# Kernel optimization log

Measured on AMD Instinct MI355X. Metric: run time of the kernel, lower is better.

Reference implementation:

```python
import jax, jax.numpy as jnp
import numpy as np

B, K, C = 8, 16384, 256
NPROP, NSAMPLE, RADIUS = 1024, 16, 0.3
NUM_CLASS, NH, NS = 18, 12, 18
DOUT = 2 + 3 + NH * 2 + NS * 4 + NUM_CLASS  # 119


def setup_inputs() -> dict:
    key = jax.random.key(0)
    ks = jax.random.split(key, 16)
    w = lambda k, shape: jax.random.normal(k, shape, jnp.float32) * 0.05
    return {
        "xyz": jax.random.uniform(ks[0], (B, K, 3), jnp.float32) * 4.0,
        "features": jax.random.normal(ks[1], (B, C, K), jnp.float32),
        # SA shared-MLP (conv2d 1x1) weights, BN folded to scale/bias (inference)
        "W1": w(ks[2], (128, C + 3)), "g1": jnp.ones((128,), jnp.float32), "b1": jnp.zeros((128,), jnp.float32),
        "W2": w(ks[3], (128, 128)),   "g2": jnp.ones((128,), jnp.float32), "b2": jnp.zeros((128,), jnp.float32),
        "W3": w(ks[4], (128, 128)),   "g3": jnp.ones((128,), jnp.float32), "b3": jnp.zeros((128,), jnp.float32),
        # proposal head conv1d stack
        "P1": w(ks[5], (128, 128)),  "pg1": jnp.ones((128,), jnp.float32), "pb1": jnp.zeros((128,), jnp.float32),
        "P2": w(ks[6], (128, 128)),  "pg2": jnp.ones((128,), jnp.float32), "pb2": jnp.zeros((128,), jnp.float32),
        "P3": w(ks[7], (DOUT, 128)), "pb3": jnp.zeros((DOUT,), jnp.float32),
        "mean_size_arr": jnp.abs(jax.random.normal(ks[8], (NS, 3), jnp.float32)) + 0.5,
    }


def fps(xyz, npoint):
    """Farthest point sampling. xyz: [B,K,3] -> [B,npoint] int32."""
    Bn, Kn, _ = xyz.shape
    def step(carry, _):
        dist, far = carry                                   # [B,K], [B]
        sel = jnp.take_along_axis(xyz, far[:, None, None], axis=1)  # [B,1,3]
        d = jnp.sum((xyz - sel) ** 2, axis=-1)              # [B,K]
        dist = jnp.minimum(dist, d)
        return (dist, jnp.argmax(dist, axis=-1).astype(jnp.int32)), far
    init = (jnp.full((Bn, Kn), 1e10, xyz.dtype), jnp.zeros((Bn,), jnp.int32))
    _, inds = jax.lax.scan(step, init, None, length=npoint)  # [npoint,B]
    return inds.T


def ball_query(new_xyz, xyz, radius, nsample):
    """First nsample points within radius of each center (pad with first hit)."""
    Kn = xyz.shape[1]
    d2 = jnp.sum((new_xyz[:, :, None, :] - xyz[:, None, :, :]) ** 2, axis=-1)  # [B,P,K]
    idx = jnp.where(d2 < radius * radius, jnp.arange(Kn, dtype=jnp.int32)[None, None, :], Kn)
    idx = jnp.sort(idx, axis=-1)[..., :nsample]             # first hits in index order
    first = idx[..., :1]                                    # center itself is always a hit
    return jnp.where(idx == Kn, first, idx).astype(jnp.int32)


def reference(xyz, features, W1, g1, b1, W2, g2, b2, W3, g3, b3,
              P1, pg1, pb1, P2, pg2, pb2, P3, pb3, mean_size_arr):
    Bn = xyz.shape[0]
    fps_idx = fps(xyz, NPROP)                                           # [B,P]
    new_xyz = jnp.take_along_axis(xyz, fps_idx[:, :, None], axis=1)     # [B,P,3]
    idx = ball_query(new_xyz, xyz, RADIUS, NSAMPLE)                     # [B,P,S]
    flat = idx.reshape(Bn, -1)
    g_xyz = jnp.take_along_axis(xyz, flat[:, :, None], axis=1).reshape(Bn, NPROP, NSAMPLE, 3)
    g_xyz = (g_xyz - new_xyz[:, :, None, :]) / RADIUS                   # normalize_xyz=True
    f = jnp.swapaxes(features, 1, 2)                                    # [B,K,C]
    g_feat = jnp.take_along_axis(f, flat[:, :, None], axis=1).reshape(Bn, NPROP, NSAMPLE, C)
    x = jnp.concatenate([g_xyz, g_feat], axis=-1)                       # [B,P,S,C+3] (use_xyz)
    for Wl, gl, bl in ((W1, g1, b1), (W2, g2, b2), (W3, g3, b3)):
        x = jax.nn.relu(jnp.einsum('bpsc,oc->bpso', x, Wl) * gl + bl)
    feat = jnp.max(x, axis=2)                                           # [B,P,128] max-pool over ball
    h = jax.nn.relu(jnp.einsum('bpc,oc->bpo', feat, P1) * pg1 + pb1)
    h = jax.nn.relu(jnp.einsum('bpc,oc->bpo', h, P2) * pg2 + pb2)
    net = jnp.einsum('bpc,oc->bpo', h, P3) + pb3                        # [B,P,119]
    # decode_scores slicing
    obj = net[:, :, 0:2]
    center = new_xyz + net[:, :, 2:5]
    heading_scores = net[:, :, 5:5 + NH]
    heading_residuals = net[:, :, 5 + NH:5 + 2 * NH] * (np.pi / NH)
    size_scores = net[:, :, 5 + 2 * NH:5 + 2 * NH + NS]
    srn = net[:, :, 5 + 2 * NH + NS:5 + 2 * NH + 4 * NS].reshape(Bn, NPROP, NS, 3)
    size_residuals = srn * mean_size_arr[None, None]
    sem_cls_scores = net[:, :, 5 + 2 * NH + 4 * NS:]
    return (obj, center, heading_scores, heading_residuals, size_scores,
            size_residuals, sem_cls_scores, feat)
```

## Files before the change

### kernel.cpp

```cpp
#include <hip/hip_runtime.h>
#include <math.h>

static constexpr int BB = 8;
static constexpr int KK = 16384;
static constexpr int CC = 256;
static constexpr int NPROP = 1024;
static constexpr int NSAMP = 16;
static constexpr int NH = 12;
static constexpr int NS = 18;
static constexpr int NCLS = 18;
static constexpr int DOUT = 119;
static constexpr int NTT = 8192;
static constexpr int NPREP = 112;

static constexpr int OFF_OBJ = 0;
static constexpr int OFF_CEN = OFF_OBJ + BB * NPROP * 2;
static constexpr int OFF_HS  = OFF_CEN + BB * NPROP * 3;
static constexpr int OFF_HR  = OFF_HS + BB * NPROP * NH;
static constexpr int OFF_SS  = OFF_HR + BB * NPROP * NH;
static constexpr int OFF_SR  = OFF_SS + BB * NPROP * NS;
static constexpr int OFF_SC  = OFF_SR + BB * NPROP * NS * 3;
static constexpr int OFF_FEAT = OFF_SC + BB * NPROP * NCLS;

__global__ __launch_bounds__(1024, 1) void stage1(
    const float* __restrict__ xyz, const float* __restrict__ features,
    const float* __restrict__ W1, const float* __restrict__ W2, const float* __restrict__ W3,
    const float* __restrict__ P1, const float* __restrict__ P2, const float* __restrict__ P3,
    float* __restrict__ fT, float* __restrict__ W1T, float* __restrict__ W2T,
    float* __restrict__ W3T, float* __restrict__ P1T, float* __restrict__ P2T,
    float* __restrict__ P3T, float* __restrict__ new_xyz) {
#pragma clang fp contract(off)
    __shared__ union {
        float t[64 * 65];
        struct { float redv[32]; int redi[32]; } r;
    } sm;
    int tid = threadIdx.x;
    int blk = blockIdx.x;

    if (blk < BB) {
        const int b = blk;
        const int lane = tid & 63, wid = tid >> 6;
        const float* xb = xyz + (size_t)b * KK * 3;

        float px[16], py[16], pz[16], dist[16];
#pragma unroll
        for (int j = 0; j < 16; j++) {
            int idx = j * 1024 + tid;
            px[j] = xb[idx * 3 + 0];
            py[j] = xb[idx * 3 + 1];
            pz[j] = xb[idx * 3 + 2];
            dist[j] = 1e10f;
        }
        float sx = xb[0], sy = xb[1], sz = xb[2];
        for (int t = 0; t < NPROP; t++) {
            if (tid == 0) {
                size_t o = ((size_t)b * NPROP + t) * 3;
                new_xyz[o + 0] = sx;
                new_xyz[o + 1] = sy;
                new_xyz[o + 2] = sz;
            }
            asm volatile("" : "+v"(px[0]), "+v"(px[1]), "+v"(px[2]), "+v"(px[3]),
                             "+v"(px[4]), "+v"(px[5]), "+v"(px[6]), "+v"(px[7]));
            asm volatile("" : "+v"(px[8]), "+v"(px[9]), "+v"(px[10]), "+v"(px[11]),
                             "+v"(px[12]), "+v"(px[13]), "+v"(px[14]), "+v"(px[15]));
            asm volatile("" : "+v"(py[0]), "+v"(py[1]), "+v"(py[2]), "+v"(py[3]),
                             "+v"(py[4]), "+v"(py[5]), "+v"(py[6]), "+v"(py[7]));
            asm volatile("" : "+v"(py[8]), "+v"(py[9]), "+v"(py[10]), "+v"(py[11]),
                             "+v"(py[12]), "+v"(py[13]), "+v"(py[14]), "+v"(py[15]));
            asm volatile("" : "+v"(pz[0]), "+v"(pz[1]), "+v"(pz[2]), "+v"(pz[3]),
                             "+v"(pz[4]), "+v"(pz[5]), "+v"(pz[6]), "+v"(pz[7]));
            asm volatile("" : "+v"(pz[8]), "+v"(pz[9]), "+v"(pz[10]), "+v"(pz[11]),
                             "+v"(pz[12]), "+v"(pz[13]), "+v"(pz[14]), "+v"(pz[15]));
            float lmax = -1.f;
            int lidx = 0;
#pragma unroll
            for (int j = 0; j < 16; j++) {
                float dx = px[j] - sx;
                float dy = py[j] - sy;
                float dz = pz[j] - sz;
                float a = dx * dx;
                float bq = dy * dy;
                float cq = dz * dz;
                float d = (a + bq) + cq;
                float nd = dist[j] < d ? dist[j] : d;
                dist[j] = nd;
                if (nd > lmax) { lmax = nd; lidx = j * 1024 + tid; }
            }
#pragma unroll
            for (int m = 1; m < 64; m <<= 1) {
                float ov = __shfl_xor(lmax, m, 64);
                int oi = __shfl_xor(lidx, m, 64);
                if (ov > lmax || (ov == lmax && oi < lidx)) { lmax = ov; lidx = oi; }
            }
            int buf = (t & 1) * 16;
            if (lane == 0) { sm.r.redv[buf + wid] = lmax; sm.r.redi[buf + wid] = lidx; }
            __syncthreads();
            float v = sm.r.redv[buf + (lane & 15)];
            int i2 = sm.r.redi[buf + (lane & 15)];
#pragma unroll
            for (int m = 1; m < 16; m <<= 1) {
                float ov = __shfl_xor(v, m, 64);
                int oi = __shfl_xor(i2, m, 64);
                if (ov > v || (ov == v && oi < i2)) { v = ov; i2 = oi; }
            }
            int cs = __builtin_amdgcn_readfirstlane(i2);
            sx = xb[cs * 3 + 0];
            sy = xb[cs * 3 + 1];
            sz = xb[cs * 3 + 2];
        }
        return;
    }
    blk -= BB;

    if (blk < NTT) {
        int bz = blk >> 10;
        int t2 = blk & 1023;
        int k0 = (t2 & 255) << 6;
        int c0 = (t2 >> 8) << 6;
        int tx = tid & 63, ty = tid >> 6;
        const float* fb = features + (size_t)bz * CC * KK;
#pragma unroll
        for (int i = 0; i < 4; i++) {
            int c = ty + (i << 4);
            sm.t[c * 65 + tx] = fb[(size_t)(c0 + c) * KK + k0 + tx];
        }
        __syncthreads();
        float* fTb = fT + (size_t)bz * KK * CC;
#pragma unroll
        for (int i = 0; i < 4; i++) {
            int k = ty + (i << 4);
            fTb[(size_t)(k0 + k) * CC + c0 + tx] = sm.t[tx * 65 + k];
        }
        return;
    }
    blk -= NTT;

    {
        int i = blk * 1024 + tid;
        if (i < 260 * 128) {
            int c = i >> 7, o = i & 127;
            W1T[i] = (c < 259) ? W1[o * 259 + c] : 0.f;
            return;
        }
        i -= 260 * 128;
        if (i < 16384) { int c = i >> 7, o = i & 127; W2T[i] = W2[o * 128 + c]; return; }
        i -= 16384;
        if (i < 16384) { int c = i >> 7, o = i & 127; W3T[i] = W3[o * 128 + c]; return; }
        i -= 16384;
        if (i < 16384) { int c = i >> 7, o = i & 127; P1T[i] = P1[o * 128 + c]; return; }
        i -= 16384;
        if (i < 16384) { int c = i >> 7, o = i & 127; P2T[i] = P2[o * 128 + c]; return; }
        i -= 16384;
        if (i < 128 * DOUT) { int c = i / DOUT, o = i % DOUT; P3T[i] = P3[o * 128 + c]; return; }
    }
}

__global__ __launch_bounds__(256) void ballquery_kernel(const float* __restrict__ xyz,
                                                        const float* __restrict__ new_xyz,
                                                        int* __restrict__ bq) {
#pragma clang fp contract(off)
    int gid = blockIdx.x * 4 + (threadIdx.x >> 6);
    int lane = threadIdx.x & 63;
    int b = gid >> 10, p = gid & 1023;
    const float* xb = xyz + (size_t)b * KK * 3;
    float cx = new_xyz[(b * NPROP + p) * 3 + 0];
    float cy = new_xyz[(b * NPROP + p) * 3 + 1];
    float cz = new_xyz[(b * NPROP + p) * 3 + 2];
    const float R2 = (float)(0.3 * 0.3);
    int out_base = (b * NPROP + p) * NSAMP;
    int found = 0;
    int firsthit = -1;
    for (int base = 0; base < KK && found < NSAMP; base += 64) {
        int k = base + lane;
        float dx = cx - xb[k * 3 + 0];
        float dy = cy - xb[k * 3 + 1];
        float dz = cz - xb[k * 3 + 2];
        float a = dx * dx;
        float bb2 = dy * dy;
        float cc2 = dz * dz;
        float d2 = (a + bb2) + cc2;
        bool pred = d2 < R2;
        unsigned long long mask = __ballot(pred);
        int prefix = __popcll(mask & ((1ull << lane) - 1ull));
        if (pred) {
            int pos = found + prefix;
            if (pos < NSAMP) bq[out_base + pos] = k;
        }
        if (firsthit < 0 && mask) firsthit = base + (__ffsll(mask) - 1);
        found += __popcll(mask);
    }
    if (lane < NSAMP && lane >= found) bq[out_base + lane] = firsthit;
}

__global__ __launch_bounds__(256) void fused_mlp(
    const float* __restrict__ fT, const float* __restrict__ xyz,
    const float* __restrict__ new_xyz, const int* __restrict__ bq,
    const float* __restrict__ W1T, const float* __restrict__ g1, const float* __restrict__ b1,
    const float* __restrict__ W2T, const float* __restrict__ g2, const float* __restrict__ b2,
    const float* __restrict__ W3T, const float* __restrict__ g3, const float* __restrict__ b3,
    const float* __restrict__ P1T, const float* __restrict__ pg1, const float* __restrict__ pb1,
    const float* __restrict__ P2T, const float* __restrict__ pg2, const float* __restrict__ pb2,
    const float* __restrict__ P3T, const float* __restrict__ pb3, const float* __restrict__ msa,
    float* __restrict__ out) {
    __shared__ float xs[16][260];
    __shared__ float hA[16][128];
    __shared__ float hB[16][128];
    __shared__ float pmax[8][128];
    __shared__ float featl[128];
    __shared__ float heada[128];
    __shared__ float headb[128];
    __shared__ int sidx[16];

    int tid = threadIdx.x;
    int blk = blockIdx.x;
    int b = blk >> 10, p = blk & 1023;
    int bp = b * NPROP + p;

    if (tid < 16) sidx[tid] = bq[bp * NSAMP + tid];
    float c0 = new_xyz[bp * 3 + 0];
    float c1 = new_xyz[bp * 3 + 1];
    float c2 = new_xyz[bp * 3 + 2];
    __syncthreads();

    for (int s = 0; s < 16; s++) {
        int k = sidx[s];
        xs[s][3 + tid] = fT[((size_t)(b * KK + k)) * CC + tid];
        if (tid < 3) {
            float xv = xyz[((size_t)(b * KK + k)) * 3 + tid];
            float cv = (tid == 0) ? c0 : (tid == 1) ? c1 : c2;
            xs[s][tid] = (xv - cv) / 0.3f;
        }
        if (tid == 3) xs[s][259] = 0.f;
    }
    __syncthreads();

    int og = tid & 31, sg = tid >> 5;
    int o0 = og * 4, s0 = sg * 2;
    float acc[4][2];

#pragma unroll
    for (int oi = 0; oi < 4; oi++) { acc[oi][0] = 0.f; acc[oi][1] = 0.f; }
    for (int cg = 0; cg < 65; cg++) {
        int cb = cg * 4;
        float wv[4][4], xv[2][4];
#pragma unroll
        for (int j = 0; j < 4; j++)
            *(float4*)&wv[j][0] = *(const float4*)&W1T[(cb + j) * 128 + o0];
        *(float4*)&xv[0][0] = *(const float4*)&xs[s0][cb];
        *(float4*)&xv[1][0] = *(const float4*)&xs[s0 + 1][cb];
#pragma unroll
        for (int j = 0; j < 4; j++)
#pragma unroll
            for (int oi = 0; oi < 4; oi++) {
                acc[oi][0] += wv[j][oi] * xv[0][j];
                acc[oi][1] += wv[j][oi] * xv[1][j];
            }
    }
    {
        float ga[4], ba[4];
        *(float4*)ga = *(const float4*)&g1[o0];
        *(float4*)ba = *(const float4*)&b1[o0];
#pragma unroll
        for (int si = 0; si < 2; si++) {
            float tmp[4];
#pragma unroll
            for (int oi = 0; oi < 4; oi++)
                tmp[oi] = fmaxf(acc[oi][si] * ga[oi] + ba[oi], 0.f);
            *(float4*)&hA[s0 + si][o0] = *(float4*)tmp;
        }
    }
    __syncthreads();

#pragma unroll
    for (int oi = 0; oi < 4; oi++) { acc[oi][0] = 0.f; acc[oi][1] = 0.f; }
    for (int cg = 0; cg < 32; cg++) {
        int cb = cg * 4;
        float wv[4][4], xv[2][4];
#pragma unroll
        for (int j = 0; j < 4; j++)
            *(float4*)&wv[j][0] = *(const float4*)&W2T[(cb + j) * 128 + o0];
        *(float4*)&xv[0][0] = *(const float4*)&hA[s0][cb];
        *(float4*)&xv[1][0] = *(const float4*)&hA[s0 + 1][cb];
#pragma unroll
        for (int j = 0; j < 4; j++)
#pragma unroll
            for (int oi = 0; oi < 4; oi++) {
                acc[oi][0] += wv[j][oi] * xv[0][j];
                acc[oi][1] += wv[j][oi] * xv[1][j];
            }
    }
    {
        float ga[4], ba[4];
        *(float4*)ga = *(const float4*)&g2[o0];
        *(float4*)ba = *(const float4*)&b2[o0];
#pragma unroll
        for (int si = 0; si < 2; si++) {
            float tmp[4];
#pragma unroll
            for (int oi = 0; oi < 4; oi++)
                tmp[oi] = fmaxf(acc[oi][si] * ga[oi] + ba[oi], 0.f);
            *(float4*)&hB[s0 + si][o0] = *(float4*)tmp;
        }
    }
    __syncthreads();

#pragma unroll
    for (int oi = 0; oi < 4; oi++) { acc[oi][0] = 0.f; acc[oi][1] = 0.f; }
    for (int cg = 0; cg < 32; cg++) {
        int cb = cg * 4;
        float wv[4][4], xv[2][4];
#pragma unroll
        for (int j = 0; j < 4; j++)
            *(float4*)&wv[j][0] = *(const float4*)&W3T[(cb + j) * 128 + o0];
        *(float4*)&xv[0][0] = *(const float4*)&hB[s0][cb];
        *(float4*)&xv[1][0] = *(const float4*)&hB[s0 + 1][cb];
#pragma unroll
        for (int j = 0; j < 4; j++)
#pragma unroll
            for (int oi = 0; oi < 4; oi++) {
                acc[oi][0] += wv[j][oi] * xv[0][j];
                acc[oi][1] += wv[j][oi] * xv[1][j];
            }
    }
    {
        float ga[4], ba[4];
        *(float4*)ga = *(const float4*)&g3[o0];
        *(float4*)ba = *(const float4*)&b3[o0];
        float tmp[4];
#pragma unroll
        for (int oi = 0; oi < 4; oi++) {
            float v0 = fmaxf(acc[oi][0] * ga[oi] + ba[oi], 0.f);
            float v1 = fmaxf(acc[oi][1] * ga[oi] + ba[oi], 0.f);
            tmp[oi] = fmaxf(v0, v1);
        }
        *(float4*)&pmax[sg][o0] = *(float4*)tmp;
    }
    __syncthreads();

    if (tid < 128) {
        float m = pmax[0][tid];
#pragma unroll
        for (int s = 1; s < 8; s++) m = fmaxf(m, pmax[s][tid]);
        featl[tid] = m;
        out[OFF_FEAT + (size_t)bp * 128 + tid] = m;
    }
    __syncthreads();

    if (tid < 128) {
        float s = 0.f;
        for (int c = 0; c < 128; c++) s += P1T[c * 128 + tid] * featl[c];
        heada[tid] = fmaxf(s * pg1[tid] + pb1[tid], 0.f);
    }
    __syncthreads();
    if (tid < 128) {
        float s = 0.f;
        for (int c = 0; c < 128; c++) s += P2T[c * 128 + tid] * heada[c];
        headb[tid] = fmaxf(s * pg2[tid] + pb2[tid], 0.f);
    }
    __syncthreads();
    if (tid < DOUT) {
        float s = 0.f;
        for (int c = 0; c < 128; c++) s += P3T[c * DOUT + tid] * headb[c];
        s += pb3[tid];
        if (tid < 2) {
            out[OFF_OBJ + (size_t)bp * 2 + tid] = s;
        } else if (tid < 5) {
            out[OFF_CEN + (size_t)bp * 3 + (tid - 2)] = new_xyz[bp * 3 + (tid - 2)] + s;
        } else if (tid < 17) {
            out[OFF_HS + (size_t)bp * NH + (tid - 5)] = s;
        } else if (tid < 29) {
            out[OFF_HR + (size_t)bp * NH + (tid - 17)] = s * (float)(M_PI / 12.0);
        } else if (tid < 47) {
            out[OFF_SS + (size_t)bp * NS + (tid - 29)] = s;
        } else if (tid < 101) {
            int j = tid - 47;
            out[OFF_SR + (size_t)bp * NS * 3 + j] = s * msa[j];
        } else {
            out[OFF_SC + (size_t)bp * NCLS + (tid - 101)] = s;
        }
    }
}

extern "C" void kernel_launch(void* const* d_in, const int* in_sizes, int n_in,
                              void* d_out, int out_size, void* d_ws, size_t ws_size,
                              hipStream_t stream) {
    const float* xyz = (const float*)d_in[0];
    const float* features = (const float*)d_in[1];
    const float* W1 = (const float*)d_in[2];
    const float* g1 = (const float*)d_in[3];
    const float* b1 = (const float*)d_in[4];
    const float* W2 = (const float*)d_in[5];
    const float* g2 = (const float*)d_in[6];
    const float* b2 = (const float*)d_in[7];
    const float* W3 = (const float*)d_in[8];
    const float* g3 = (const float*)d_in[9];
    const float* b3 = (const float*)d_in[10];
    const float* P1 = (const float*)d_in[11];
    const float* pg1 = (const float*)d_in[12];
    const float* pb1 = (const float*)d_in[13];
    const float* P2 = (const float*)d_in[14];
    const float* pg2 = (const float*)d_in[15];
    const float* pb2 = (const float*)d_in[16];
    const float* P3 = (const float*)d_in[17];
    const float* pb3 = (const float*)d_in[18];
    const float* msa = (const float*)d_in[19];
    float* out = (float*)d_out;

    char* w = (char*)d_ws;
    float* W1T = (float*)w; w += (size_t)260 * 128 * 4;
    float* W2T = (float*)w; w += 16384 * 4;
    float* W3T = (float*)w; w += 16384 * 4;
    float* P1T = (float*)w; w += 16384 * 4;
    float* P2T = (float*)w; w += 16384 * 4;
    float* P3T = (float*)w; w += 16384 * 4;
    float* nxyz = (float*)w; w += (size_t)BB * NPROP * 3 * 4;
    int* bq = (int*)w;     w += (size_t)BB * NPROP * NSAMP * 4;
    float* fT = (float*)w; w += (size_t)BB * KK * CC * 4;

    stage1<<<BB + NTT + NPREP, 1024, 0, stream>>>(
        xyz, features, W1, W2, W3, P1, P2, P3,
        fT, W1T, W2T, W3T, P1T, P2T, P3T, nxyz);
    ballquery_kernel<<<(BB * NPROP) / 4, 256, 0, stream>>>(xyz, nxyz, bq);
    fused_mlp<<<BB * NPROP, 256, 0, stream>>>(
        fT, xyz, nxyz, bq,
        W1T, g1, b1, W2T, g2, b2, W3T, g3, b3,
        P1T, pg1, pb1, P2T, pg2, pb2, P3T, pb3, msa, out);
}
```

Baseline: 3.588 ms.

## Split farthest point sampling across cooperative blocks with global barriers

```diff
diff --git a/kernel.cpp b/kernel.cpp
--- a/kernel.cpp
+++ b/kernel.cpp
@@ -13,6 +13,9 @@
 static constexpr int NTT = 8192;
 static constexpr int NPREP = 112;
 
+static constexpr int SUBS = 8;
+static constexpr int FPT = 8;
+
 static constexpr int OFF_OBJ = 0;
 static constexpr int OFF_CEN = OFF_OBJ + BB * NPROP * 2;
 static constexpr int OFF_HS  = OFF_CEN + BB * NPROP * 3;
@@ -22,95 +25,115 @@
 static constexpr int OFF_SC  = OFF_SR + BB * NPROP * NS * 3;
 static constexpr int OFF_FEAT = OFF_SC + BB * NPROP * NCLS;
 
-__global__ __launch_bounds__(1024, 1) void stage1(
-    const float* __restrict__ xyz, const float* __restrict__ features,
+__global__ __launch_bounds__(256) void fps_coop(
+    const float* __restrict__ xyz, float* __restrict__ new_xyz,
+    unsigned* __restrict__ bar, unsigned long long* __restrict__ rec) {
+#pragma clang fp contract(off)
+    __shared__ unsigned long long rp[8];
+    int tid = threadIdx.x;
+    int bid = blockIdx.x;
+    int batch = bid >> 3, sub = bid & 7;
+    int lane = tid & 63, wid = tid >> 6;
+    const float* xb = xyz + (size_t)batch * KK * 3;
+    int pbase = sub * 2048 + tid;
+
+    float px[FPT], py[FPT], pz[FPT], dst[FPT];
+#pragma unroll
+    for (int j = 0; j < FPT; j++) {
+        int p = pbase + j * 256;
+        px[j] = xb[p * 3 + 0];
+        py[j] = xb[p * 3 + 1];
+        pz[j] = xb[p * 3 + 2];
+        dst[j] = 1e10f;
+    }
+    float sx = xb[0], sy = xb[1], sz = xb[2];
+    unsigned* mybar = bar + batch * 16;
+
+    for (int t = 0; t < NPROP; t++) {
+        if (sub == 0 && tid == 0) {
+            size_t o = ((size_t)batch * NPROP + t) * 3;
+            new_xyz[o + 0] = sx;
+            new_xyz[o + 1] = sy;
+            new_xyz[o + 2] = sz;
+        }
+        asm volatile("" : "+v"(px[0]), "+v"(px[1]), "+v"(px[2]), "+v"(px[3]),
+                         "+v"(px[4]), "+v"(px[5]), "+v"(px[6]), "+v"(px[7]));
+        asm volatile("" : "+v"(py[0]), "+v"(py[1]), "+v"(py[2]), "+v"(py[3]),
+                         "+v"(py[4]), "+v"(py[5]), "+v"(py[6]), "+v"(py[7]));
+        asm volatile("" : "+v"(pz[0]), "+v"(pz[1]), "+v"(pz[2]), "+v"(pz[3]),
+                         "+v"(pz[4]), "+v"(pz[5]), "+v"(pz[6]), "+v"(pz[7]));
+        float lmax = -1.f;
+        int lidx = 0;
+#pragma unroll
+        for (int j = 0; j < FPT; j++) {
+            float dx = px[j] - sx;
+            float dy = py[j] - sy;
+            float dz = pz[j] - sz;
+            float a = dx * dx;
+            float bq = dy * dy;
+            float cq = dz * dz;
+            float d = (a + bq) + cq;
+            float nd = dst[j] < d ? dst[j] : d;
+            dst[j] = nd;
+            if (nd > lmax) { lmax = nd; lidx = pbase + j * 256; }
+        }
+        unsigned long long mypack =
+            ((unsigned long long)__builtin_bit_cast(unsigned, lmax) << 32) |
+            (unsigned)~lidx;
+        unsigned long long bp = mypack;
+#pragma unroll
+        for (int m = 1; m < 64; m <<= 1) {
+            unsigned long long o = __shfl_xor(bp, m, 64);
+            if (o > bp) bp = o;
+        }
+        int buf = (t & 1) * 4;
+        if (lane == 0) rp[buf + wid] = bp;
+        __syncthreads();
+        unsigned long long blockbest = rp[buf + 0];
+#pragma unroll
+        for (int s = 1; s < 4; s++)
+            if (rp[buf + s] > blockbest) blockbest = rp[buf + s];
+        if (mypack == blockbest) {
+            __hip_atomic_store(&rec[(t & 1) * 64 + batch * 8 + sub], blockbest,
+                               __ATOMIC_RELAXED, __HIP_MEMORY_SCOPE_AGENT);
+        }
+        __syncthreads();
+        if (tid == 0) {
+            __threadfence();
+            __hip_atomic_fetch_add(mybar, 1u, __ATOMIC_RELEASE,
+                                   __HIP_MEMORY_SCOPE_AGENT);
+            unsigned tgt = 8u * (unsigned)(t + 1);
+            while (__hip_atomic_load(mybar, __ATOMIC_ACQUIRE,
+                                     __HIP_MEMORY_SCOPE_AGENT) < tgt)
+                __builtin_amdgcn_s_sleep(1);
+        }
+        __syncthreads();
+        unsigned long long* rb = rec + (t & 1) * 64 + batch * 8;
+        unsigned long long best = __hip_atomic_load(&rb[0], __ATOMIC_RELAXED,
+                                                    __HIP_MEMORY_SCOPE_AGENT);
+#pragma unroll
+        for (int s = 1; s < 8; s++) {
+            unsigned long long q = __hip_atomic_load(&rb[s], __ATOMIC_RELAXED,
+                                                     __HIP_MEMORY_SCOPE_AGENT);
+            if (q > best) best = q;
+        }
+        int cs = (int)~(unsigned)(best & 0xffffffffull);
+        sx = xb[cs * 3 + 0];
+        sy = xb[cs * 3 + 1];
+        sz = xb[cs * 3 + 2];
+    }
+}
+
+__global__ __launch_bounds__(1024) void prep_transpose(
+    const float* __restrict__ features,
     const float* __restrict__ W1, const float* __restrict__ W2, const float* __restrict__ W3,
     const float* __restrict__ P1, const float* __restrict__ P2, const float* __restrict__ P3,
     float* __restrict__ fT, float* __restrict__ W1T, float* __restrict__ W2T,
     float* __restrict__ W3T, float* __restrict__ P1T, float* __restrict__ P2T,
-    float* __restrict__ P3T, float* __restrict__ new_xyz) {
-#pragma clang fp contract(off)
-    __shared__ union {
-        float t[64 * 65];
-        struct { float redv[32]; int redi[32]; } r;
-    } sm;
+    float* __restrict__ P3T) {
+    __shared__ float sm[64 * 65];
     int tid = threadIdx.x;
     int blk = blockIdx.x;
-
-    if (blk < BB) {
-        const int b = blk;
-        const int lane = tid & 63, wid = tid >> 6;
-        const float* xb = xyz + (size_t)b * KK * 3;
-
-        float px[16], py[16], pz[16], dist[16];
-#pragma unroll
-        for (int j = 0; j < 16; j++) {
-            int idx = j * 1024 + tid;
-            px[j] = xb[idx * 3 + 0];
-            py[j] = xb[idx * 3 + 1];
-            pz[j] = xb[idx * 3 + 2];
-            dist[j] = 1e10f;
-        }
-        float sx = xb[0], sy = xb[1], sz = xb[2];
-        for (int t = 0; t < NPROP; t++) {
-            if (tid == 0) {
-                size_t o = ((size_t)b * NPROP + t) * 3;
-                new_xyz[o + 0] = sx;
-                new_xyz[o + 1] = sy;
-                new_xyz[o + 2] = sz;
-            }
-            asm volatile("" : "+v"(px[0]), "+v"(px[1]), "+v"(px[2]), "+v"(px[3]),
-                             "+v"(px[4]), "+v"(px[5]), "+v"(px[6]), "+v"(px[7]));
-            asm volatile("" : "+v"(px[8]), "+v"(px[9]), "+v"(px[10]), "+v"(px[11]),
-                             "+v"(px[12]), "+v"(px[13]), "+v"(px[14]), "+v"(px[15]));
-            asm volatile("" : "+v"(py[0]), "+v"(py[1]), "+v"(py[2]), "+v"(py[3]),
-                             "+v"(py[4]), "+v"(py[5]), "+v"(py[6]), "+v"(py[7]));
-            asm volatile("" : "+v"(py[8]), "+v"(py[9]), "+v"(py[10]), "+v"(py[11]),
-                             "+v"(py[12]), "+v"(py[13]), "+v"(py[14]), "+v"(py[15]));
-            asm volatile("" : "+v"(pz[0]), "+v"(pz[1]), "+v"(pz[2]), "+v"(pz[3]),
-                             "+v"(pz[4]), "+v"(pz[5]), "+v"(pz[6]), "+v"(pz[7]));
-            asm volatile("" : "+v"(pz[8]), "+v"(pz[9]), "+v"(pz[10]), "+v"(pz[11]),
-                             "+v"(pz[12]), "+v"(pz[13]), "+v"(pz[14]), "+v"(pz[15]));
-            float lmax = -1.f;
-            int lidx = 0;
-#pragma unroll
-            for (int j = 0; j < 16; j++) {
-                float dx = px[j] - sx;
-                float dy = py[j] - sy;
-                float dz = pz[j] - sz;
-                float a = dx * dx;
-                float bq = dy * dy;
-                float cq = dz * dz;
-                float d = (a + bq) + cq;
-                float nd = dist[j] < d ? dist[j] : d;
-                dist[j] = nd;
-                if (nd > lmax) { lmax = nd; lidx = j * 1024 + tid; }
-            }
-#pragma unroll
-            for (int m = 1; m < 64; m <<= 1) {
-                float ov = __shfl_xor(lmax, m, 64);
-                int oi = __shfl_xor(lidx, m, 64);
-                if (ov > lmax || (ov == lmax && oi < lidx)) { lmax = ov; lidx = oi; }
-            }
-            int buf = (t & 1) * 16;
-            if (lane == 0) { sm.r.redv[buf + wid] = lmax; sm.r.redi[buf + wid] = lidx; }
-            __syncthreads();
-            float v = sm.r.redv[buf + (lane & 15)];
-            int i2 = sm.r.redi[buf + (lane & 15)];
-#pragma unroll
-            for (int m = 1; m < 16; m <<= 1) {
-                float ov = __shfl_xor(v, m, 64);
-                int oi = __shfl_xor(i2, m, 64);
-                if (ov > v || (ov == v && oi < i2)) { v = ov; i2 = oi; }
-            }
-            int cs = __builtin_amdgcn_readfirstlane(i2);
-            sx = xb[cs * 3 + 0];
-            sy = xb[cs * 3 + 1];
-            sz = xb[cs * 3 + 2];
-        }
-        return;
-    }
-    blk -= BB;
 
     if (blk < NTT) {
         int bz = blk >> 10;
@@ -122,19 +145,18 @@
 #pragma unroll
         for (int i = 0; i < 4; i++) {
             int c = ty + (i << 4);
-            sm.t[c * 65 + tx] = fb[(size_t)(c0 + c) * KK + k0 + tx];
+            sm[c * 65 + tx] = fb[(size_t)(c0 + c) * KK + k0 + tx];
         }
         __syncthreads();
         float* fTb = fT + (size_t)bz * KK * CC;
 #pragma unroll
         for (int i = 0; i < 4; i++) {
             int k = ty + (i << 4);
-            fTb[(size_t)(k0 + k) * CC + c0 + tx] = sm.t[tx * 65 + k];
+            fTb[(size_t)(k0 + k) * CC + c0 + tx] = sm[tx * 65 + k];
         }
         return;
     }
     blk -= NTT;
-
     {
         int i = blk * 1024 + tid;
         if (i < 260 * 128) {
@@ -407,6 +429,9 @@
     float* out = (float*)d_out;
 
     char* w = (char*)d_ws;
+    unsigned* bar = (unsigned*)w;             w += 512;
+    unsigned long long* rec = (unsigned long long*)w; w += 1024;
+    w += 2560;
     float* W1T = (float*)w; w += (size_t)260 * 128 * 4;
     float* W2T = (float*)w; w += 16384 * 4;
     float* W3T = (float*)w; w += 16384 * 4;
@@ -417,9 +442,15 @@
     int* bq = (int*)w;     w += (size_t)BB * NPROP * NSAMP * 4;
     float* fT = (float*)w; w += (size_t)BB * KK * CC * 4;
 
-    stage1<<<BB + NTT + NPREP, 1024, 0, stream>>>(
-        xyz, features, W1, W2, W3, P1, P2, P3,
-        fT, W1T, W2T, W3T, P1T, P2T, P3T, nxyz);
+    hipMemsetAsync(bar, 0, 512, stream);
+
+    void* fps_args[] = {(void*)&xyz, (void*)&nxyz, (void*)&bar, (void*)&rec};
+    hipLaunchCooperativeKernel((void*)fps_coop, dim3(BB * SUBS), dim3(256),
+                               fps_args, 0, stream);
+
+    prep_transpose<<<NTT + NPREP, 1024, 0, stream>>>(
+        features, W1, W2, W3, P1, P2, P3,
+        fT, W1T, W2T, W3T, P1T, P2T, P3T);
     ballquery_kernel<<<(BB * NPROP) / 4, 256, 0, stream>>>(xyz, nxyz, bq);
     fused_mlp<<<BB * NPROP, 256, 0, stream>>>(
         fT, xyz, nxyz, bq,
```

New measurement: 4.329 ms. 1.21x slower.
